# Kernel optimization log

Measured on AMD Instinct MI355X. Metric: run time of the kernel, lower is better.

## Reference

```python
import jax, jax.numpy as jnp
import numpy as np

D_IN = 1024
D_OUT = 1024
SEQ = 2048
BATCH = 4


def setup_inputs() -> dict:
    key = jax.random.key(0)
    ks = jax.random.split(key, 7)
    s_in = 1.0 / np.sqrt(D_IN)
    return {
        "x": jax.random.normal(ks[0], (BATCH, SEQ, D_IN), dtype=jnp.float32),
        "Wq": jax.random.normal(ks[1], (D_IN, D_OUT), dtype=jnp.float32) * s_in,
        "bq": jax.random.normal(ks[2], (D_OUT,), dtype=jnp.float32) * 0.01,
        "Wk": jax.random.normal(ks[3], (D_IN, D_OUT), dtype=jnp.float32) * s_in,
        "bk": jax.random.normal(ks[4], (D_OUT,), dtype=jnp.float32) * 0.01,
        "Wv": jax.random.normal(ks[5], (D_IN, D_OUT), dtype=jnp.float32) * s_in,
        "bv": jax.random.normal(ks[6], (D_OUT,), dtype=jnp.float32) * 0.01,
    }


def reference(x, Wq, bq, Wk, bk, Wv, bv):
    # x: [b, n, d_in]
    b, n, d_in = x.shape
    q = x @ Wq + bq  # [b, n, d_out]
    k = x @ Wk + bk
    v = x @ Wv + bv
    scale = 1.0 / jnp.sqrt(jnp.asarray(d_in, x.dtype))
    scores = jnp.einsum("bqd,bkd->bqk", q, k) * scale  # [b, n, n]
    causal = jnp.triu(jnp.ones((n, n), dtype=bool), k=1)  # True above diagonal
    scores = jnp.where(causal, -jnp.inf, scores)
    weights = jax.nn.softmax(scores, axis=-1)
    # dropout p=0.0 -> identity
    context = jnp.einsum("bqk,bkd->bqd", weights, v)
    return context
```

## Files before the change

### kernel.cpp

```cpp
#include <hip/hip_runtime.h>

typedef unsigned short u16;
typedef __bf16 bf16x8 __attribute__((ext_vector_type(8)));
typedef float floatx4 __attribute__((ext_vector_type(4)));

#define B_ 4
#define SEQ 2048
#define DIM 1024

__device__ __forceinline__ u16 f2bf(float f) {
    unsigned u = __builtin_bit_cast(unsigned, f);
    u += 0x7FFFu + ((u >> 16) & 1u);
    return (u16)(u >> 16);
}
__device__ __forceinline__ float bf2f(u16 h) {
    unsigned u = ((unsigned)h) << 16;
    return __builtin_bit_cast(float, u);
}

#define GPTR(p) ((const __attribute__((address_space(1))) void*)(p))
#define LPTR(p) ((__attribute__((address_space(3))) void*)(p))

__global__ __launch_bounds__(256) void convert_x(const float4* __restrict__ x,
                                                 ushort4* __restrict__ xb) {
    int i = blockIdx.x * 256 + threadIdx.x;
    float4 v = x[i];
    ushort4 o;
    o.x = f2bf(v.x); o.y = f2bf(v.y); o.z = f2bf(v.z); o.w = f2bf(v.w);
    xb[i] = o;
}

__global__ __launch_bounds__(256) void transpose_w(const float* __restrict__ Wq,
                                                   const float* __restrict__ Wk,
                                                   const float* __restrict__ Wv,
                                                   u16* __restrict__ Wt) {
    __shared__ u16 t[64][66];
    const int z = blockIdx.z;
    const float* W = (z == 0) ? Wq : ((z == 1) ? Wk : Wv);
    u16* out = Wt + (size_t)z * DIM * DIM;
    const int tx = threadIdx.x, ty = threadIdx.y;
    const int k0 = blockIdx.x * 64, n0 = blockIdx.y * 64;
#pragma unroll
    for (int j = 0; j < 8; j++) {
        int k = ty + 8 * j;
        float2 v = *(const float2*)(W + (size_t)(k0 + k) * DIM + n0 + 2 * tx);
        t[2 * tx][k] = f2bf(v.x);
        t[2 * tx + 1][k] = f2bf(v.y);
    }
    __syncthreads();
#pragma unroll
    for (int j = 0; j < 8; j++) {
        int n = ty + 8 * j;
        ushort2 o;
        o.x = t[n][2 * tx];
        o.y = t[n][2 * tx + 1];
        *(ushort2*)(out + (size_t)(n0 + n) * DIM + k0 + 2 * tx) = o;
    }
}

__device__ __forceinline__ void run_mainloop(
    const u16* __restrict__ Ab, const u16* __restrict__ Bb, int lda, int ldb,
    int Kt, u16* lsA, u16* lsB, int tid, int wave, int quad, int l15,
    int wm, int wn, floatx4 (&acc)[4][4]) {
    const int srow = tid >> 2;
    const int scol = (tid & 3) * 8;
    const u16* gA0 = Ab + (size_t)srow * lda + scol;
    const u16* gA1 = gA0 + (size_t)64 * lda;
    const u16* gB0 = Bb + (size_t)srow * ldb + scol;
    const u16* gB1 = gB0 + (size_t)64 * ldb;
    u16* lA0 = lsA + wave * 512;
    u16* lA1 = lsA + 2048 + wave * 512;
    u16* lB0 = lsB + wave * 512;
    u16* lB1 = lsB + 2048 + wave * 512;

#pragma unroll
    for (int i = 0; i < 4; i++)
#pragma unroll
        for (int j = 0; j < 4; j++) {
            floatx4 zz = {0.f, 0.f, 0.f, 0.f};
            acc[i][j] = zz;
        }

    for (int k0 = 0; k0 < Kt; k0 += 32) {
        __builtin_amdgcn_global_load_lds(GPTR(gA0), LPTR(lA0), 16, 0, 0);
        __builtin_amdgcn_global_load_lds(GPTR(gA1), LPTR(lA1), 16, 0, 0);
        __builtin_amdgcn_global_load_lds(GPTR(gB0), LPTR(lB0), 16, 0, 0);
        __builtin_amdgcn_global_load_lds(GPTR(gB1), LPTR(lB1), 16, 0, 0);
        gA0 += 32; gA1 += 32; gB0 += 32; gB1 += 32;
        __syncthreads();

        bf16x8 af[4], bfr[4];
#pragma unroll
        for (int i = 0; i < 4; i++) {
            af[i] = *(const bf16x8*)(lsA + (wm + i * 16 + l15) * 32 + quad * 8);
            bfr[i] = *(const bf16x8*)(lsB + (wn + i * 16 + l15) * 32 + quad * 8);
        }
#pragma unroll
        for (int i = 0; i < 4; i++)
#pragma unroll
            for (int j = 0; j < 4; j++)
                acc[i][j] = __builtin_amdgcn_mfma_f32_16x16x32_bf16(af[i], bfr[j], acc[i][j], 0, 0, 0);
        __syncthreads();
    }
}

__global__ __launch_bounds__(256) void gemm_qkv(
    const u16* __restrict__ A, const u16* __restrict__ Bt, u16* __restrict__ QK,
    const float* __restrict__ b0, const float* __restrict__ b1, const float* __restrict__ b2,
    u16* __restrict__ VtOut) {
    __shared__ union {
        u16 stage[2][128 * 32];
        u16 epT[128 * 72];
    } sm;
    const int tid = threadIdx.x;
    const int wave = tid >> 6, lane = tid & 63;
    const int quad = lane >> 4, l15 = lane & 15;
    const int wm = (wave >> 1) * 64, wn = (wave & 1) * 64;
    const int z = blockIdx.z, yb = blockIdx.y;

    const u16* Ab = A + (size_t)yb * 128 * DIM;
    const u16* Bb = Bt + (size_t)z * DIM * DIM + (size_t)blockIdx.x * 128 * DIM;
    floatx4 acc[4][4];
    run_mainloop(Ab, Bb, DIM, DIM, DIM, sm.stage[0], sm.stage[1],
                 tid, wave, quad, l15, wm, wn, acc);

    const int colbase = blockIdx.x * 128;
    const int mq = quad * 4;
    const float* bias = (z == 0) ? b0 : ((z == 1) ? b1 : b2);
    const int n0 = colbase + wn + l15;

    if (z < 2) {
        u16* Cb = QK + (size_t)z * B_ * SEQ * DIM;
        const int m0 = yb * 128 + wm + mq;
#pragma unroll
        for (int j = 0; j < 4; j++) {
            float bv_ = bias[n0 + j * 16];
#pragma unroll
            for (int i = 0; i < 4; i++)
#pragma unroll
                for (int r = 0; r < 4; r++)
                    Cb[(size_t)(m0 + i * 16 + r) * DIM + (n0 + j * 16)] = f2bf(acc[i][j][r] + bv_);
        }
        return;
    }

    float addj[4];
#pragma unroll
    for (int j = 0; j < 4; j++) addj[j] = bias[n0 + j * 16];
#pragma unroll
    for (int c = 0; c < 2; c++) {
        __syncthreads();
        if ((wave >> 1) == c) {
#pragma unroll
            for (int i = 0; i < 4; i++)
#pragma unroll
                for (int j = 0; j < 4; j++)
#pragma unroll
                    for (int r = 0; r < 4; r++) {
                        int lr = i * 16 + mq + r;
                        int lc = wn + j * 16 + l15;
                        sm.epT[lc * 72 + lr] = f2bf(acc[i][j][r] + addj[j]);
                    }
        }
        __syncthreads();
        int gm0 = yb * 128 + c * 64;
        int b = gm0 >> 11;
        int sb = gm0 & (SEQ - 1);
        u16* Vb = VtOut + (size_t)b * DIM * SEQ;
#pragma unroll
        for (int k = 0; k < 4; k++) {
            int s2 = tid + 256 * k;
            int n = s2 >> 3, seg = s2 & 7;
            uint4 val = *(const uint4*)&sm.epT[n * 72 + seg * 8];
            *(uint4*)(Vb + (size_t)(colbase + n) * SEQ + sb + seg * 8) = val;
        }
    }
}

__global__ __launch_bounds__(256) void gemm_scores(
    const u16* __restrict__ Q, const u16* __restrict__ K, u16* __restrict__ S,
    float scale) {
    const int yb = gridDim.y - 1 - blockIdx.y;
    if ((int)blockIdx.x > yb) return;

    __shared__ u16 stage[2][128 * 32];
    const int tid = threadIdx.x;
    const int wave = tid >> 6, lane = tid & 63;
    const int quad = lane >> 4, l15 = lane & 15;
    const int wm = (wave >> 1) * 64, wn = (wave & 1) * 64;
    const int z = blockIdx.z;

    const u16* Ab = Q + (size_t)z * SEQ * DIM + (size_t)yb * 128 * DIM;
    const u16* Bb = K + (size_t)z * SEQ * DIM + (size_t)blockIdx.x * 128 * DIM;
    floatx4 acc[4][4];
    run_mainloop(Ab, Bb, DIM, DIM, DIM, stage[0], stage[1],
                 tid, wave, quad, l15, wm, wn, acc);

    u16* Cb = S + (size_t)z * SEQ * SEQ;
    const int m0 = yb * 128 + wm + quad * 4;
    const int n0 = blockIdx.x * 128 + wn + l15;
#pragma unroll
    for (int j = 0; j < 4; j++)
#pragma unroll
        for (int i = 0; i < 4; i++)
#pragma unroll
            for (int r = 0; r < 4; r++)
                Cb[(size_t)(m0 + i * 16 + r) * SEQ + (n0 + j * 16)] = f2bf(acc[i][j][r] * scale);
}

__global__ __launch_bounds__(256) void gemm_pv(
    const u16* __restrict__ P, const u16* __restrict__ Vt, float* __restrict__ O) {
    const int yb = gridDim.y - 1 - blockIdx.y;
    __shared__ u16 stage[2][128 * 32];
    const int tid = threadIdx.x;
    const int wave = tid >> 6, lane = tid & 63;
    const int quad = lane >> 4, l15 = lane & 15;
    const int wm = (wave >> 1) * 64, wn = (wave & 1) * 64;
    const int z = blockIdx.z;

    const u16* Ab = P + (size_t)z * SEQ * SEQ + (size_t)yb * 128 * SEQ;
    const u16* Bb = Vt + (size_t)z * DIM * SEQ + (size_t)blockIdx.x * 128 * SEQ;
    const int Kt = (yb + 1) * 128;
    floatx4 acc[4][4];
    run_mainloop(Ab, Bb, SEQ, SEQ, Kt, stage[0], stage[1],
                 tid, wave, quad, l15, wm, wn, acc);

    float* Cf = O + (size_t)z * SEQ * DIM;
    const int m0 = yb * 128 + wm + quad * 4;
    const int n0 = blockIdx.x * 128 + wn + l15;
#pragma unroll
    for (int j = 0; j < 4; j++)
#pragma unroll
        for (int i = 0; i < 4; i++)
#pragma unroll
            for (int r = 0; r < 4; r++)
                Cf[(size_t)(m0 + i * 16 + r) * DIM + (n0 + j * 16)] = acc[i][j][r];
}

__global__ __launch_bounds__(256) void softmax_causal(u16* __restrict__ S) {
    const int q = blockIdx.x, b = blockIdx.y, tid = threadIdx.x;
    u16* row = S + ((size_t)b * SEQ + q) * SEQ;
    const int L = q + 1;
    const int Z = ((q >> 7) + 1) << 7;
    const int k0 = tid * 8;
    __shared__ float redm[4], reds[4];

    uint4 rv = ((const uint4*)row)[tid];
    unsigned w[4] = {rv.x, rv.y, rv.z, rv.w};
    float f[8];
#pragma unroll
    for (int e = 0; e < 8; e++) {
        u16 h = (u16)((w[e >> 1] >> ((e & 1) * 16)) & 0xFFFFu);
        f[e] = (k0 + e < L) ? bf2f(h) : -3.0e38f;
    }
    float m = f[0];
#pragma unroll
    for (int e = 1; e < 8; e++) m = fmaxf(m, f[e]);
#pragma unroll
    for (int o = 32; o > 0; o >>= 1) m = fmaxf(m, __shfl_xor(m, o));
    if ((tid & 63) == 0) redm[tid >> 6] = m;
    __syncthreads();
    m = fmaxf(fmaxf(redm[0], redm[1]), fmaxf(redm[2], redm[3]));

    float p[8];
    float s = 0.f;
#pragma unroll
    for (int e = 0; e < 8; e++) {
        p[e] = (k0 + e < L) ? __expf(f[e] - m) : 0.f;
        s += p[e];
    }
#pragma unroll
    for (int o = 32; o > 0; o >>= 1) s += __shfl_xor(s, o);
    if ((tid & 63) == 0) reds[tid >> 6] = s;
    __syncthreads();
    s = reds[0] + reds[1] + reds[2] + reds[3];
    const float inv = 1.0f / s;

    if (k0 < Z) {
        unsigned o2[4];
#pragma unroll
        for (int e = 0; e < 4; e++) {
            unsigned lo = f2bf(p[2 * e] * inv);
            unsigned hi = f2bf(p[2 * e + 1] * inv);
            o2[e] = lo | (hi << 16);
        }
        uint4 ov = {o2[0], o2[1], o2[2], o2[3]};
        ((uint4*)row)[tid] = ov;
    }
}

extern "C" void kernel_launch(void* const* d_in, const int* in_sizes, int n_in,
                              void* d_out, int out_size, void* d_ws, size_t ws_size,
                              hipStream_t stream) {
    const float* x = (const float*)d_in[0];
    const float* Wq = (const float*)d_in[1];
    const float* bq = (const float*)d_in[2];
    const float* Wk = (const float*)d_in[3];
    const float* bk = (const float*)d_in[4];
    const float* Wv = (const float*)d_in[5];
    const float* bv = (const float*)d_in[6];
    float* out = (float*)d_out;

    char* ws = (char*)d_ws;
    const size_t MB = 1024ull * 1024ull;
    u16* S = (u16*)ws;
    u16* xb = (u16*)ws;
    u16* Wt = (u16*)(ws + 16 * MB);
    u16* QK = (u16*)(ws + 32 * MB);
    u16* Vt = (u16*)(ws + 64 * MB);
    const size_t MAT = (size_t)B_ * SEQ * DIM;
    u16* Q = QK;
    u16* Km = QK + MAT;

    const float scale = 0.03125f;

    convert_x<<<8192, 256, 0, stream>>>((const float4*)x, (ushort4*)xb);
    transpose_w<<<dim3(16, 16, 3), dim3(32, 8), 0, stream>>>(Wq, Wk, Wv, Wt);
    gemm_qkv<<<dim3(8, 64, 3), 256, 0, stream>>>(xb, Wt, QK, bq, bk, bv, Vt);
    gemm_scores<<<dim3(16, 16, 4), 256, 0, stream>>>(Q, Km, S, scale);
    softmax_causal<<<dim3(SEQ, B_), 256, 0, stream>>>(S);
    gemm_pv<<<dim3(8, 16, 4), 256, 0, stream>>>(S, Vt, out);
}
```

Baseline: 293.9 us.

## Use K=64 mainloop steps, 64-row tiles for attention GEMMs, flatten QKV grid

The GEMM mainloop now loads a 64-wide K slice per iteration as two 32-wide halves, which halves the number of barrier pairs per K. The scores and PV GEMMs switch to 64x128 output tiles so causal skipping happens at a finer grain and more blocks are available. The QKV GEMM grid folds the three weight matrices into blockIdx.x so blocks sharing the same x rows are scheduled together. The cost is more LDS per block, less reuse per block for the attention GEMMs, and more blocks to launch.

```diff
diff --git a/kernel.cpp b/kernel.cpp
--- a/kernel.cpp
+++ b/kernel.cpp
@@ -58,20 +58,16 @@
     }
 }
 
-__device__ __forceinline__ void run_mainloop(
+template <int TM>
+__device__ __forceinline__ void mainloop64(
     const u16* __restrict__ Ab, const u16* __restrict__ Bb, int lda, int ldb,
     int Kt, u16* lsA, u16* lsB, int tid, int wave, int quad, int l15,
     int wm, int wn, floatx4 (&acc)[4][4]) {
+    const int AI = TM / 32;
     const int srow = tid >> 2;
     const int scol = (tid & 3) * 8;
-    const u16* gA0 = Ab + (size_t)srow * lda + scol;
-    const u16* gA1 = gA0 + (size_t)64 * lda;
-    const u16* gB0 = Bb + (size_t)srow * ldb + scol;
-    const u16* gB1 = gB0 + (size_t)64 * ldb;
-    u16* lA0 = lsA + wave * 512;
-    u16* lA1 = lsA + 2048 + wave * 512;
-    u16* lB0 = lsB + wave * 512;
-    u16* lB1 = lsB + 2048 + wave * 512;
+    const u16* gA = Ab + (size_t)srow * lda + scol;
+    const u16* gB = Bb + (size_t)srow * ldb + scol;
 
 #pragma unroll
     for (int i = 0; i < 4; i++)
@@ -81,25 +77,44 @@
             acc[i][j] = zz;
         }
 
-    for (int k0 = 0; k0 < Kt; k0 += 32) {
-        __builtin_amdgcn_global_load_lds(GPTR(gA0), LPTR(lA0), 16, 0, 0);
-        __builtin_amdgcn_global_load_lds(GPTR(gA1), LPTR(lA1), 16, 0, 0);
-        __builtin_amdgcn_global_load_lds(GPTR(gB0), LPTR(lB0), 16, 0, 0);
-        __builtin_amdgcn_global_load_lds(GPTR(gB1), LPTR(lB1), 16, 0, 0);
-        gA0 += 32; gA1 += 32; gB0 += 32; gB1 += 32;
+    for (int k0 = 0; k0 < Kt; k0 += 64) {
+#pragma unroll
+        for (int h = 0; h < 2; h++) {
+            if (TM == 128) {
+#pragma unroll
+                for (int c = 0; c < 2; c++)
+                    __builtin_amdgcn_global_load_lds(
+                        GPTR(gA + (size_t)c * 64 * lda + h * 32),
+                        LPTR(lsA + h * 4096 + c * 2048 + wave * 512), 16, 0, 0);
+            } else {
+                __builtin_amdgcn_global_load_lds(
+                    GPTR(gA + h * 32),
+                    LPTR(lsA + h * 2048 + wave * 512), 16, 0, 0);
+            }
+#pragma unroll
+            for (int c = 0; c < 2; c++)
+                __builtin_amdgcn_global_load_lds(
+                    GPTR(gB + (size_t)c * 64 * ldb + h * 32),
+                    LPTR(lsB + h * 4096 + c * 2048 + wave * 512), 16, 0, 0);
+        }
+        gA += 64; gB += 64;
         __syncthreads();
 
-        bf16x8 af[4], bfr[4];
-#pragma unroll
-        for (int i = 0; i < 4; i++) {
-            af[i] = *(const bf16x8*)(lsA + (wm + i * 16 + l15) * 32 + quad * 8);
-            bfr[i] = *(const bf16x8*)(lsB + (wn + i * 16 + l15) * 32 + quad * 8);
-        }
-#pragma unroll
-        for (int i = 0; i < 4; i++)
+#pragma unroll
+        for (int h = 0; h < 2; h++) {
+            bf16x8 af[AI], bfr[4];
+#pragma unroll
+            for (int i = 0; i < AI; i++)
+                af[i] = *(const bf16x8*)(lsA + h * (TM * 32) + (wm + i * 16 + l15) * 32 + quad * 8);
 #pragma unroll
             for (int j = 0; j < 4; j++)
-                acc[i][j] = __builtin_amdgcn_mfma_f32_16x16x32_bf16(af[i], bfr[j], acc[i][j], 0, 0, 0);
+                bfr[j] = *(const bf16x8*)(lsB + h * 4096 + (wn + j * 16 + l15) * 32 + quad * 8);
+#pragma unroll
+            for (int i = 0; i < AI; i++)
+#pragma unroll
+                for (int j = 0; j < 4; j++)
+                    acc[i][j] = __builtin_amdgcn_mfma_f32_16x16x32_bf16(af[i], bfr[j], acc[i][j], 0, 0, 0);
+        }
         __syncthreads();
     }
 }
@@ -109,22 +124,22 @@
     const float* __restrict__ b0, const float* __restrict__ b1, const float* __restrict__ b2,
     u16* __restrict__ VtOut) {
     __shared__ union {
-        u16 stage[2][128 * 32];
+        u16 stage[2][128 * 64];
         u16 epT[128 * 72];
     } sm;
     const int tid = threadIdx.x;
     const int wave = tid >> 6, lane = tid & 63;
     const int quad = lane >> 4, l15 = lane & 15;
     const int wm = (wave >> 1) * 64, wn = (wave & 1) * 64;
-    const int z = blockIdx.z, yb = blockIdx.y;
+    const int z = blockIdx.x >> 3, xb8 = blockIdx.x & 7, yb = blockIdx.y;
 
     const u16* Ab = A + (size_t)yb * 128 * DIM;
-    const u16* Bb = Bt + (size_t)z * DIM * DIM + (size_t)blockIdx.x * 128 * DIM;
+    const u16* Bb = Bt + (size_t)z * DIM * DIM + (size_t)xb8 * 128 * DIM;
     floatx4 acc[4][4];
-    run_mainloop(Ab, Bb, DIM, DIM, DIM, sm.stage[0], sm.stage[1],
-                 tid, wave, quad, l15, wm, wn, acc);
-
-    const int colbase = blockIdx.x * 128;
+    mainloop64<128>(Ab, Bb, DIM, DIM, DIM, sm.stage[0], sm.stage[1],
+                    tid, wave, quad, l15, wm, wn, acc);
+
+    const int colbase = xb8 * 128;
     const int mq = quad * 4;
     const float* bias = (z == 0) ? b0 : ((z == 1) ? b1 : b2);
     const int n0 = colbase + wn + l15;
@@ -180,29 +195,30 @@
 __global__ __launch_bounds__(256) void gemm_scores(
     const u16* __restrict__ Q, const u16* __restrict__ K, u16* __restrict__ S,
     float scale) {
-    const int yb = gridDim.y - 1 - blockIdx.y;
-    if ((int)blockIdx.x > yb) return;
-
-    __shared__ u16 stage[2][128 * 32];
+    const int ym = gridDim.y - 1 - blockIdx.y;
+    if ((int)blockIdx.x > (ym >> 1)) return;
+
+    __shared__ u16 lsA[64 * 64];
+    __shared__ u16 lsB[128 * 64];
     const int tid = threadIdx.x;
     const int wave = tid >> 6, lane = tid & 63;
     const int quad = lane >> 4, l15 = lane & 15;
-    const int wm = (wave >> 1) * 64, wn = (wave & 1) * 64;
+    const int wm = (wave >> 1) * 32, wn = (wave & 1) * 64;
     const int z = blockIdx.z;
 
-    const u16* Ab = Q + (size_t)z * SEQ * DIM + (size_t)yb * 128 * DIM;
+    const u16* Ab = Q + (size_t)z * SEQ * DIM + (size_t)ym * 64 * DIM;
     const u16* Bb = K + (size_t)z * SEQ * DIM + (size_t)blockIdx.x * 128 * DIM;
     floatx4 acc[4][4];
-    run_mainloop(Ab, Bb, DIM, DIM, DIM, stage[0], stage[1],
-                 tid, wave, quad, l15, wm, wn, acc);
+    mainloop64<64>(Ab, Bb, DIM, DIM, DIM, lsA, lsB,
+                   tid, wave, quad, l15, wm, wn, acc);
 
     u16* Cb = S + (size_t)z * SEQ * SEQ;
-    const int m0 = yb * 128 + wm + quad * 4;
+    const int m0 = ym * 64 + wm + quad * 4;
     const int n0 = blockIdx.x * 128 + wn + l15;
 #pragma unroll
     for (int j = 0; j < 4; j++)
 #pragma unroll
-        for (int i = 0; i < 4; i++)
+        for (int i = 0; i < 2; i++)
 #pragma unroll
             for (int r = 0; r < 4; r++)
                 Cb[(size_t)(m0 + i * 16 + r) * SEQ + (n0 + j * 16)] = f2bf(acc[i][j][r] * scale);
@@ -210,28 +226,29 @@
 
 __global__ __launch_bounds__(256) void gemm_pv(
     const u16* __restrict__ P, const u16* __restrict__ Vt, float* __restrict__ O) {
-    const int yb = gridDim.y - 1 - blockIdx.y;
-    __shared__ u16 stage[2][128 * 32];
+    const int ym = gridDim.y - 1 - blockIdx.y;
+    __shared__ u16 lsA[64 * 64];
+    __shared__ u16 lsB[128 * 64];
     const int tid = threadIdx.x;
     const int wave = tid >> 6, lane = tid & 63;
     const int quad = lane >> 4, l15 = lane & 15;
-    const int wm = (wave >> 1) * 64, wn = (wave & 1) * 64;
+    const int wm = (wave >> 1) * 32, wn = (wave & 1) * 64;
     const int z = blockIdx.z;
 
-    const u16* Ab = P + (size_t)z * SEQ * SEQ + (size_t)yb * 128 * SEQ;
+    const u16* Ab = P + (size_t)z * SEQ * SEQ + (size_t)ym * 64 * SEQ;
     const u16* Bb = Vt + (size_t)z * DIM * SEQ + (size_t)blockIdx.x * 128 * SEQ;
-    const int Kt = (yb + 1) * 128;
+    const int Kt = ((ym + 2) >> 1) * 128;
     floatx4 acc[4][4];
-    run_mainloop(Ab, Bb, SEQ, SEQ, Kt, stage[0], stage[1],
-                 tid, wave, quad, l15, wm, wn, acc);
+    mainloop64<64>(Ab, Bb, SEQ, SEQ, Kt, lsA, lsB,
+                   tid, wave, quad, l15, wm, wn, acc);
 
     float* Cf = O + (size_t)z * SEQ * DIM;
-    const int m0 = yb * 128 + wm + quad * 4;
+    const int m0 = ym * 64 + wm + quad * 4;
     const int n0 = blockIdx.x * 128 + wn + l15;
 #pragma unroll
     for (int j = 0; j < 4; j++)
 #pragma unroll
-        for (int i = 0; i < 4; i++)
+        for (int i = 0; i < 2; i++)
 #pragma unroll
             for (int r = 0; r < 4; r++)
                 Cf[(size_t)(m0 + i * 16 + r) * DIM + (n0 + j * 16)] = acc[i][j][r];
@@ -316,8 +333,8 @@
 
     convert_x<<<8192, 256, 0, stream>>>((const float4*)x, (ushort4*)xb);
     transpose_w<<<dim3(16, 16, 3), dim3(32, 8), 0, stream>>>(Wq, Wk, Wv, Wt);
-    gemm_qkv<<<dim3(8, 64, 3), 256, 0, stream>>>(xb, Wt, QK, bq, bk, bv, Vt);
-    gemm_scores<<<dim3(16, 16, 4), 256, 0, stream>>>(Q, Km, S, scale);
+    gemm_qkv<<<dim3(24, 64), 256, 0, stream>>>(xb, Wt, QK, bq, bk, bv, Vt);
+    gemm_scores<<<dim3(16, 32, 4), 256, 0, stream>>>(Q, Km, S, scale);
     softmax_causal<<<dim3(SEQ, B_), 256, 0, stream>>>(S);
-    gemm_pv<<<dim3(8, 16, 4), 256, 0, stream>>>(S, Vt, out);
-}
+    gemm_pv<<<dim3(8, 32, 4), 256, 0, stream>>>(S, Vt, out);
+}
```

Result: faster. 275.7 us (-6.2%).

## Shrink GEMM tiles to 128x64 with K=64 steps and reorganize grids

Applied to the files above, without the earlier changes.

All three GEMMs switch from 128x128 output tiles with K-step 32 to 128x64 tiles with K-step 64, which halves the accumulator registers and the number of barriers per K. Launch bounds request 4 blocks per CU, and grids double along N to fill more CUs. The QKV grid folds the projection index into blockIdx.x, and the V-transpose epilogue becomes a single pass. The trade-off is less reuse of each loaded A tile per MFMA and more total global traffic, in exchange for better occupancy and finer causal skipping.

```diff
diff --git a/kernel.cpp b/kernel.cpp
--- a/kernel.cpp
+++ b/kernel.cpp
@@ -58,73 +58,76 @@
     }
 }
 
-__device__ __forceinline__ void run_mainloop(
+__device__ __forceinline__ void mainloop(
     const u16* __restrict__ Ab, const u16* __restrict__ Bb, int lda, int ldb,
     int Kt, u16* lsA, u16* lsB, int tid, int wave, int quad, int l15,
-    int wm, int wn, floatx4 (&acc)[4][4]) {
+    int wm, int wn, floatx4 (&acc)[4][2]) {
     const int srow = tid >> 2;
     const int scol = (tid & 3) * 8;
-    const u16* gA0 = Ab + (size_t)srow * lda + scol;
-    const u16* gA1 = gA0 + (size_t)64 * lda;
-    const u16* gB0 = Bb + (size_t)srow * ldb + scol;
-    const u16* gB1 = gB0 + (size_t)64 * ldb;
-    u16* lA0 = lsA + wave * 512;
-    u16* lA1 = lsA + 2048 + wave * 512;
-    u16* lB0 = lsB + wave * 512;
-    u16* lB1 = lsB + 2048 + wave * 512;
+    const u16* gA = Ab + (size_t)srow * lda + scol;
+    const u16* gB = Bb + (size_t)srow * ldb + scol;
 
 #pragma unroll
     for (int i = 0; i < 4; i++)
 #pragma unroll
-        for (int j = 0; j < 4; j++) {
+        for (int j = 0; j < 2; j++) {
             floatx4 zz = {0.f, 0.f, 0.f, 0.f};
             acc[i][j] = zz;
         }
 
-    for (int k0 = 0; k0 < Kt; k0 += 32) {
-        __builtin_amdgcn_global_load_lds(GPTR(gA0), LPTR(lA0), 16, 0, 0);
-        __builtin_amdgcn_global_load_lds(GPTR(gA1), LPTR(lA1), 16, 0, 0);
-        __builtin_amdgcn_global_load_lds(GPTR(gB0), LPTR(lB0), 16, 0, 0);
-        __builtin_amdgcn_global_load_lds(GPTR(gB1), LPTR(lB1), 16, 0, 0);
-        gA0 += 32; gA1 += 32; gB0 += 32; gB1 += 32;
+    for (int k0 = 0; k0 < Kt; k0 += 64) {
+#pragma unroll
+        for (int h = 0; h < 2; h++) {
+            __builtin_amdgcn_global_load_lds(GPTR(gA + h * 32),
+                LPTR(lsA + h * 4096 + wave * 512), 16, 0, 0);
+            __builtin_amdgcn_global_load_lds(GPTR(gA + (size_t)64 * lda + h * 32),
+                LPTR(lsA + h * 4096 + 2048 + wave * 512), 16, 0, 0);
+            __builtin_amdgcn_global_load_lds(GPTR(gB + h * 32),
+                LPTR(lsB + h * 2048 + wave * 512), 16, 0, 0);
+        }
+        gA += 64; gB += 64;
         __syncthreads();
 
-        bf16x8 af[4], bfr[4];
-#pragma unroll
-        for (int i = 0; i < 4; i++) {
-            af[i] = *(const bf16x8*)(lsA + (wm + i * 16 + l15) * 32 + quad * 8);
-            bfr[i] = *(const bf16x8*)(lsB + (wn + i * 16 + l15) * 32 + quad * 8);
-        }
-#pragma unroll
-        for (int i = 0; i < 4; i++)
-#pragma unroll
-            for (int j = 0; j < 4; j++)
-                acc[i][j] = __builtin_amdgcn_mfma_f32_16x16x32_bf16(af[i], bfr[j], acc[i][j], 0, 0, 0);
+#pragma unroll
+        for (int h = 0; h < 2; h++) {
+            bf16x8 af[4], bfr[2];
+#pragma unroll
+            for (int i = 0; i < 4; i++)
+                af[i] = *(const bf16x8*)(lsA + h * 4096 + (wm + i * 16 + l15) * 32 + quad * 8);
+#pragma unroll
+            for (int j = 0; j < 2; j++)
+                bfr[j] = *(const bf16x8*)(lsB + h * 2048 + (wn + j * 16 + l15) * 32 + quad * 8);
+#pragma unroll
+            for (int i = 0; i < 4; i++)
+#pragma unroll
+                for (int j = 0; j < 2; j++)
+                    acc[i][j] = __builtin_amdgcn_mfma_f32_16x16x32_bf16(af[i], bfr[j], acc[i][j], 0, 0, 0);
+        }
         __syncthreads();
     }
 }
 
-__global__ __launch_bounds__(256) void gemm_qkv(
+__global__ __launch_bounds__(256, 4) void gemm_qkv(
     const u16* __restrict__ A, const u16* __restrict__ Bt, u16* __restrict__ QK,
     const float* __restrict__ b0, const float* __restrict__ b1, const float* __restrict__ b2,
     u16* __restrict__ VtOut) {
     __shared__ union {
-        u16 stage[2][128 * 32];
-        u16 epT[128 * 72];
+        struct { u16 a[128 * 64]; u16 b[64 * 64]; } stage;
+        u16 epT[64 * 136];
     } sm;
     const int tid = threadIdx.x;
     const int wave = tid >> 6, lane = tid & 63;
     const int quad = lane >> 4, l15 = lane & 15;
-    const int wm = (wave >> 1) * 64, wn = (wave & 1) * 64;
-    const int z = blockIdx.z, yb = blockIdx.y;
+    const int wm = (wave >> 1) * 64, wn = (wave & 1) * 32;
+    const int z = blockIdx.x >> 4, xn = blockIdx.x & 15, yb = blockIdx.y;
 
     const u16* Ab = A + (size_t)yb * 128 * DIM;
-    const u16* Bb = Bt + (size_t)z * DIM * DIM + (size_t)blockIdx.x * 128 * DIM;
-    floatx4 acc[4][4];
-    run_mainloop(Ab, Bb, DIM, DIM, DIM, sm.stage[0], sm.stage[1],
-                 tid, wave, quad, l15, wm, wn, acc);
-
-    const int colbase = blockIdx.x * 128;
+    const u16* Bb = Bt + (size_t)z * DIM * DIM + (size_t)xn * 64 * DIM;
+    floatx4 acc[4][2];
+    mainloop(Ab, Bb, DIM, DIM, DIM, sm.stage.a, sm.stage.b,
+             tid, wave, quad, l15, wm, wn, acc);
+
+    const int colbase = xn * 64;
     const int mq = quad * 4;
     const float* bias = (z == 0) ? b0 : ((z == 1) ? b1 : b2);
     const int n0 = colbase + wn + l15;
@@ -133,7 +136,7 @@
         u16* Cb = QK + (size_t)z * B_ * SEQ * DIM;
         const int m0 = yb * 128 + wm + mq;
 #pragma unroll
-        for (int j = 0; j < 4; j++) {
+        for (int j = 0; j < 2; j++) {
             float bv_ = bias[n0 + j * 16];
 #pragma unroll
             for (int i = 0; i < 4; i++)
@@ -144,63 +147,58 @@
         return;
     }
 
-    float addj[4];
-#pragma unroll
-    for (int j = 0; j < 4; j++) addj[j] = bias[n0 + j * 16];
-#pragma unroll
-    for (int c = 0; c < 2; c++) {
-        __syncthreads();
-        if ((wave >> 1) == c) {
-#pragma unroll
-            for (int i = 0; i < 4; i++)
-#pragma unroll
-                for (int j = 0; j < 4; j++)
-#pragma unroll
-                    for (int r = 0; r < 4; r++) {
-                        int lr = i * 16 + mq + r;
-                        int lc = wn + j * 16 + l15;
-                        sm.epT[lc * 72 + lr] = f2bf(acc[i][j][r] + addj[j]);
-                    }
-        }
-        __syncthreads();
-        int gm0 = yb * 128 + c * 64;
-        int b = gm0 >> 11;
-        int sb = gm0 & (SEQ - 1);
-        u16* Vb = VtOut + (size_t)b * DIM * SEQ;
-#pragma unroll
-        for (int k = 0; k < 4; k++) {
-            int s2 = tid + 256 * k;
-            int n = s2 >> 3, seg = s2 & 7;
-            uint4 val = *(const uint4*)&sm.epT[n * 72 + seg * 8];
-            *(uint4*)(Vb + (size_t)(colbase + n) * SEQ + sb + seg * 8) = val;
-        }
-    }
-}
-
-__global__ __launch_bounds__(256) void gemm_scores(
+    float addj[2];
+#pragma unroll
+    for (int j = 0; j < 2; j++) addj[j] = bias[n0 + j * 16];
+    __syncthreads();
+#pragma unroll
+    for (int i = 0; i < 4; i++)
+#pragma unroll
+        for (int j = 0; j < 2; j++)
+#pragma unroll
+            for (int r = 0; r < 4; r++) {
+                int lr = wm + i * 16 + mq + r;
+                int lc = wn + j * 16 + l15;
+                sm.epT[lc * 136 + lr] = f2bf(acc[i][j][r] + addj[j]);
+            }
+    __syncthreads();
+    const int b = (yb * 128) >> 11;
+    const int sb = (yb * 128) & (SEQ - 1);
+    u16* Vb = VtOut + (size_t)b * DIM * SEQ;
+#pragma unroll
+    for (int k = 0; k < 4; k++) {
+        int s2 = tid + 256 * k;
+        int n = s2 >> 4, seg = s2 & 15;
+        uint4 val = *(const uint4*)&sm.epT[n * 136 + seg * 8];
+        *(uint4*)(Vb + (size_t)(colbase + n) * SEQ + sb + seg * 8) = val;
+    }
+}
+
+__global__ __launch_bounds__(256, 4) void gemm_scores(
     const u16* __restrict__ Q, const u16* __restrict__ K, u16* __restrict__ S,
     float scale) {
-    const int yb = gridDim.y - 1 - blockIdx.y;
-    if ((int)blockIdx.x > yb) return;
-
-    __shared__ u16 stage[2][128 * 32];
+    const int ym = gridDim.y - 1 - blockIdx.y;
+    if ((int)blockIdx.x > 2 * ym + 1) return;
+
+    __shared__ u16 lsA[128 * 64];
+    __shared__ u16 lsB[64 * 64];
     const int tid = threadIdx.x;
     const int wave = tid >> 6, lane = tid & 63;
     const int quad = lane >> 4, l15 = lane & 15;
-    const int wm = (wave >> 1) * 64, wn = (wave & 1) * 64;
+    const int wm = (wave >> 1) * 64, wn = (wave & 1) * 32;
     const int z = blockIdx.z;
 
-    const u16* Ab = Q + (size_t)z * SEQ * DIM + (size_t)yb * 128 * DIM;
-    const u16* Bb = K + (size_t)z * SEQ * DIM + (size_t)blockIdx.x * 128 * DIM;
-    floatx4 acc[4][4];
-    run_mainloop(Ab, Bb, DIM, DIM, DIM, stage[0], stage[1],
-                 tid, wave, quad, l15, wm, wn, acc);
+    const u16* Ab = Q + (size_t)z * SEQ * DIM + (size_t)ym * 128 * DIM;
+    const u16* Bb = K + (size_t)z * SEQ * DIM + (size_t)blockIdx.x * 64 * DIM;
+    floatx4 acc[4][2];
+    mainloop(Ab, Bb, DIM, DIM, DIM, lsA, lsB,
+             tid, wave, quad, l15, wm, wn, acc);
 
     u16* Cb = S + (size_t)z * SEQ * SEQ;
-    const int m0 = yb * 128 + wm + quad * 4;
-    const int n0 = blockIdx.x * 128 + wn + l15;
-#pragma unroll
-    for (int j = 0; j < 4; j++)
+    const int m0 = ym * 128 + wm + quad * 4;
+    const int n0 = blockIdx.x * 64 + wn + l15;
+#pragma unroll
+    for (int j = 0; j < 2; j++)
 #pragma unroll
         for (int i = 0; i < 4; i++)
 #pragma unroll
@@ -208,28 +206,29 @@
                 Cb[(size_t)(m0 + i * 16 + r) * SEQ + (n0 + j * 16)] = f2bf(acc[i][j][r] * scale);
 }
 
-__global__ __launch_bounds__(256) void gemm_pv(
+__global__ __launch_bounds__(256, 4) void gemm_pv(
     const u16* __restrict__ P, const u16* __restrict__ Vt, float* __restrict__ O) {
-    const int yb = gridDim.y - 1 - blockIdx.y;
-    __shared__ u16 stage[2][128 * 32];
+    const int ym = gridDim.y - 1 - blockIdx.y;
+    __shared__ u16 lsA[128 * 64];
+    __shared__ u16 lsB[64 * 64];
     const int tid = threadIdx.x;
     const int wave = tid >> 6, lane = tid & 63;
     const int quad = lane >> 4, l15 = lane & 15;
-    const int wm = (wave >> 1) * 64, wn = (wave & 1) * 64;
+    const int wm = (wave >> 1) * 64, wn = (wave & 1) * 32;
     const int z = blockIdx.z;
 
-    const u16* Ab = P + (size_t)z * SEQ * SEQ + (size_t)yb * 128 * SEQ;
-    const u16* Bb = Vt + (size_t)z * DIM * SEQ + (size_t)blockIdx.x * 128 * SEQ;
-    const int Kt = (yb + 1) * 128;
-    floatx4 acc[4][4];
-    run_mainloop(Ab, Bb, SEQ, SEQ, Kt, stage[0], stage[1],
-                 tid, wave, quad, l15, wm, wn, acc);
+    const u16* Ab = P + (size_t)z * SEQ * SEQ + (size_t)ym * 128 * SEQ;
+    const u16* Bb = Vt + (size_t)z * DIM * SEQ + (size_t)blockIdx.x * 64 * SEQ;
+    const int Kt = (ym + 1) * 128;
+    floatx4 acc[4][2];
+    mainloop(Ab, Bb, SEQ, SEQ, Kt, lsA, lsB,
+             tid, wave, quad, l15, wm, wn, acc);
 
     float* Cf = O + (size_t)z * SEQ * DIM;
-    const int m0 = yb * 128 + wm + quad * 4;
-    const int n0 = blockIdx.x * 128 + wn + l15;
-#pragma unroll
-    for (int j = 0; j < 4; j++)
+    const int m0 = ym * 128 + wm + quad * 4;
+    const int n0 = blockIdx.x * 64 + wn + l15;
+#pragma unroll
+    for (int j = 0; j < 2; j++)
 #pragma unroll
         for (int i = 0; i < 4; i++)
 #pragma unroll
@@ -316,8 +315,8 @@
 
     convert_x<<<8192, 256, 0, stream>>>((const float4*)x, (ushort4*)xb);
     transpose_w<<<dim3(16, 16, 3), dim3(32, 8), 0, stream>>>(Wq, Wk, Wv, Wt);
-    gemm_qkv<<<dim3(8, 64, 3), 256, 0, stream>>>(xb, Wt, QK, bq, bk, bv, Vt);
-    gemm_scores<<<dim3(16, 16, 4), 256, 0, stream>>>(Q, Km, S, scale);
+    gemm_qkv<<<dim3(48, 64), 256, 0, stream>>>(xb, Wt, QK, bq, bk, bv, Vt);
+    gemm_scores<<<dim3(32, 16, 4), 256, 0, stream>>>(Q, Km, S, scale);
     softmax_causal<<<dim3(SEQ, B_), 256, 0, stream>>>(S);
-    gemm_pv<<<dim3(8, 16, 4), 256, 0, stream>>>(S, Vt, out);
-}
+    gemm_pv<<<dim3(16, 16, 4), 256, 0, stream>>>(S, Vt, out);
+}
```

Result: faster. 282.7 us (-3.8%).
